# Kernel tuning notes

Hardware: AMD Instinct MI355X
Metric: run time of the kernel (lower is better)

The kernel has to match this reference:

```python
import math
import jax, jax.numpy as jnp
import numpy as np

T, B, E, H = 2048, 1, 2048, 32
HD = E // H          # head_dim = 64
HALF = HD // 2       # rotary half = 32
SCALE_LENGTH = 1024


def duplicate_interleave(m):
    # [S, HALF] -> [S, HD], each column duplicated adjacently
    return jnp.repeat(m, 2, axis=-1)


def rotate_every_two(x):
    # x: [BH, S, HD]
    x1 = x[:, :, ::2]
    x2 = x[:, :, 1::2]
    return jnp.stack((-x2, x1), axis=-1).reshape(x.shape)


def apply_rotary_pos_emb(x, sin, cos, scale):
    # sin/cos/scale: [S, HALF]; x: [BH, S, HD]
    sin2 = duplicate_interleave(sin * scale)
    cos2 = duplicate_interleave(cos * scale)
    return x * cos2 + rotate_every_two(x) * sin2


def setup_inputs() -> dict:
    key = jax.random.key(0)
    ks = jax.random.split(key, 8)
    std = 0.02
    query = jax.random.normal(ks[0], (T, B, E), jnp.float32)
    key_t = jax.random.normal(ks[1], (T, B, E), jnp.float32)
    value = jax.random.normal(ks[2], (T, B, E), jnp.float32)
    Wq = jax.random.normal(ks[3], (E, E), jnp.float32) * std
    Wk = jax.random.normal(ks[4], (E, E), jnp.float32) * std
    Wv = jax.random.normal(ks[5], (E, E), jnp.float32) * std
    Wo = jax.random.normal(ks[6], (E, E), jnp.float32) * std
    bq = jnp.zeros((E,), jnp.float32)
    bk = jnp.zeros((E,), jnp.float32)
    bv = jnp.zeros((E,), jnp.float32)
    bo = jnp.zeros((E,), jnp.float32)
    # XPos-style rotary tables
    pos = jnp.arange(T, dtype=jnp.float32)
    inv_freq = 1.0 / (10000.0 ** (jnp.arange(HALF, dtype=jnp.float32) / HALF))
    ang = pos[:, None] * inv_freq[None, :]          # [T, HALF]
    sin = jnp.sin(ang)
    cos = jnp.cos(ang)
    scale_base = 512.0
    dim_scale = (jnp.arange(0, HD, 2, dtype=jnp.float32) + 0.4 * HD) / (1.4 * HD)
    xscale = dim_scale[None, :] ** (pos[:, None] / scale_base)  # [T, HALF]
    # causal additive mask
    attn_mask = jnp.where(jnp.triu(jnp.ones((T, T), bool), k=1), -1e9, 0.0).astype(jnp.float32)
    return {"query": query, "key": key_t, "value": value,
            "Wq": Wq, "bq": bq, "Wk": Wk, "bk": bk, "Wv": Wv, "bv": bv,
            "Wo": Wo, "bo": bo, "sin": sin, "cos": cos, "xscale": xscale,
            "attn_mask": attn_mask, "scale_length": SCALE_LENGTH}


def reference(query, key, value, Wq, bq, Wk, bk, Wv, bv, Wo, bo,
              sin, cos, xscale, attn_mask, scale_length):
    tgt_len, bsz, embed_dim = query.shape
    scaling = HD ** -0.5

    def proj(x, W, b):
        y = x @ W.T + b                                # [T, B, E]
        return y.reshape(tgt_len, bsz * H, HD).transpose(1, 0, 2)  # [BH, T, HD]

    q = proj(query, Wq, bq)
    k = proj(key, Wk, bk)
    v = proj(value, Wv, bv)

    # self-attention XPos rotary: k scaled by 1/xscale, q by xscale (last q_len rows)
    k = apply_rotary_pos_emb(k, sin, cos, 1.0 / xscale)
    q = apply_rotary_pos_emb(q, sin[-tgt_len:], cos[-tgt_len:], xscale[-tgt_len:])

    src_len = k.shape[1]
    if src_len > scale_length:
        pos_k = jnp.arange(src_len - tgt_len, src_len, dtype=jnp.float32)
        scale_attention = jnp.maximum(1.0, jnp.log(pos_k) / math.log(scale_length))
        q = q * scale_attention[None, :, None]

    q = q * scaling
    attn_weights = jnp.einsum('btd,bsd->bts', q, k)      # [BH, T, S]
    attn_weights = attn_weights + attn_mask[None, :, :]
    attn_weights = jax.nn.softmax(attn_weights.astype(jnp.float32), axis=-1
                                  ).astype(q.dtype)
    attn = jnp.einsum('bts,bsd->btd', attn_weights, v)   # [BH, T, HD]
    attn = attn.transpose(1, 0, 2).reshape(tgt_len, bsz, embed_dim)
    attn = attn @ Wo.T + bo
    return attn
```

## Files before the change

### kernel.cpp

```cpp
#include <hip/hip_runtime.h>
#include <hip/hip_bf16.h>
#include <math.h>

#define T_LEN 2048
#define EMB   2048
#define NH    32
#define HD    64
#define HALF  32

typedef __attribute__((ext_vector_type(8))) short short8v;
typedef __attribute__((ext_vector_type(4))) float floatx4;

__device__ inline void gload_lds16(const void* g, void* l) {
    __builtin_amdgcn_global_load_lds(
        (const __attribute__((address_space(1))) unsigned int*)g,
        (__attribute__((address_space(3))) unsigned int*)l,
        16, 0, 0);
}

__device__ inline ushort f2bf(float x) {
    union { float f; unsigned u; } c; c.f = x;
    const unsigned r = c.u + 0x7FFFu + ((c.u >> 16) & 1u);
    return (ushort)(r >> 16);
}

#define BARRIER() do { asm volatile("" ::: "memory"); \
    __builtin_amdgcn_s_barrier(); asm volatile("" ::: "memory"); } while (0)
#define VMW4() asm volatile("s_waitcnt vmcnt(4)" ::: "memory")

__global__ __launch_bounds__(256) void conv_all(
    const float* __restrict__ s0, const float* __restrict__ s1,
    const float* __restrict__ s2, const float* __restrict__ s3,
    const float* __restrict__ s4, const float* __restrict__ s5,
    const float* __restrict__ s6, ushort* __restrict__ dst)
{
    const int idx = blockIdx.x * 256 + threadIdx.x;
    const int t = idx >> 19;
    const int r = (idx & 524287) * 8;
    const float* in = t == 0 ? s0 : t == 1 ? s1 : t == 2 ? s2 : t == 3 ? s3
                    : t == 4 ? s4 : t == 5 ? s5 : s6;
    const float4 v0 = *reinterpret_cast<const float4*>(&in[r]);
    const float4 v1 = *reinterpret_cast<const float4*>(&in[r + 4]);
    ushort o[8];
    o[0] = f2bf(v0.x); o[1] = f2bf(v0.y); o[2] = f2bf(v0.z); o[3] = f2bf(v0.w);
    o[4] = f2bf(v1.x); o[5] = f2bf(v1.y); o[6] = f2bf(v1.z); o[7] = f2bf(v1.w);
    *reinterpret_cast<uint4*>(&dst[(size_t)t * 4194304 + r]) =
        *reinterpret_cast<const uint4*>(o);
}

__global__ __launch_bounds__(256) void rot_tables(
    const float* __restrict__ sinp, const float* __restrict__ cosp,
    const float* __restrict__ xscale,
    float2* __restrict__ qt, float2* __restrict__ kt)
{
    const int idx = blockIdx.x * 256 + threadIdx.x;
    const int t = idx >> 5;
    const float s = sinp[idx], c = cosp[idx], xs = xscale[idx];
    float sa = 1.f;
    if (t >= 2) {
        const float lv = __logf((float)t) * 0.14426950408889634f;
        sa = lv > 1.f ? lv : 1.f;
    }
    const float qs = xs * sa * 0.125f * 1.4426950408889634f;
    qt[idx] = make_float2(c * qs, s * qs);
    const float ks = 1.f / xs;
    kt[idx] = make_float2(c * ks, s * ks);
}

#define QBM 256
#define QBN 256

#define STAGE_A(tau, h) do {                                                   \
    const int _tc = ((tau) & 31) * 64;                                         \
    _Pragma("unroll") for (int _i = 0; _i < 2; ++_i) {                         \
        gload_lds16(&Ap[(size_t)(bm + (h) * 128 + wid * 16 + _i * 8 + rl) * 2048 + _tc + csw], \
                    &lds[((tau) & 1) * 16384 + (h) * 8192 + (wid * 16 + _i * 8) * 64]); \
    } } while (0)

#define STAGE_B(tau, h) do {                                                   \
    const int _tc = ((tau) & 31) * 64;                                         \
    _Pragma("unroll") for (int _i = 0; _i < 2; ++_i) {                         \
        gload_lds16(&Bp[(size_t)(bn + (h) * 128 + wid * 16 + _i * 8 + rl) * 2048 + _tc + csw], \
                    &lds[32768 + ((tau) & 1) * 16384 + (h) * 8192 + (wid * 16 + _i * 8) * 64]); \
    } } while (0)

#define PH(slot, mp, VMWSTMT, ...) do {                                        \
    if ((mp) == 0) {                                                           \
        _Pragma("unroll") for (int n = 0; n < 4; ++n) {                        \
            bf[n][0] = ldB(slot, n, 0);                                        \
            bf[n][1] = ldB(slot, n, 1);                                        \
        }                                                                      \
    }                                                                          \
    af[0][0] = ldA(slot, (mp) * 2, 0);     af[0][1] = ldA(slot, (mp) * 2, 1);  \
    af[1][0] = ldA(slot, (mp) * 2 + 1, 0); af[1][1] = ldA(slot, (mp) * 2 + 1, 1); \
    __VA_ARGS__;                                                               \
    BARRIER();                                                                 \
    __builtin_amdgcn_s_setprio(1);                                             \
    _Pragma("unroll") for (int mm = 0; mm < 2; ++mm)                           \
    _Pragma("unroll") for (int n = 0; n < 4; ++n)                              \
    _Pragma("unroll") for (int kk = 0; kk < 2; ++kk)                           \
        acc[(mp) * 2 + mm][n] = __builtin_amdgcn_mfma_f32_16x16x32_bf16(       \
            af[mm][kk], bf[n][kk], acc[(mp) * 2 + mm][n], 0, 0, 0);            \
    __builtin_amdgcn_s_setprio(0);                                             \
    VMWSTMT;                                                                   \
    BARRIER();                                                                 \
} while (0)

__global__ __launch_bounds__(512, 2) void gemm_qkv8(
    const ushort* __restrict__ Astack,
    const ushort* __restrict__ Wstack,
    const float* __restrict__ bq, const float* __restrict__ bk,
    const float* __restrict__ bv,
    ushort* __restrict__ outQ, ushort* __restrict__ outK,
    ushort* __restrict__ outVt,
    const float2* __restrict__ qtab, const float2* __restrict__ ktab)
{
    __shared__ ushort lds[65536];
    const int tid  = threadIdx.x;
    const int lane = tid & 63;
    const int wid  = tid >> 6;

    const int b   = blockIdx.x + blockIdx.y * 24;
    const int xcd = b & 7;
    const int idx = b >> 3;
    const int bx  = xcd * 3 + (idx >> 3);
    const int by  = idx & 7;
    const int which = bx >> 3;
    const int bn  = (bx & 7) * QBN;
    const int bm  = by * QBM;
    const ushort* Ap = Astack + (size_t)which * 4194304;
    const ushort* Bp = Wstack + (size_t)which * 4194304;

    const int rl  = lane >> 3;
    const int csw = (((lane & 7) ^ ((lane >> 3) & 7)) * 8);
    const int lm  = lane & 15;
    const int lg  = lane >> 4;
    const char* ldsb = reinterpret_cast<const char*>(lds);

    auto ldA = [&](int slot, int m, int kk) -> short8v {
        const int row = m * 16 + lm;
        const int off = (slot * 16384 + (wid >> 2) * 8192) * 2 + row * 128
                      + (((kk * 4 + lg) ^ (row & 7)) * 16);
        return *reinterpret_cast<const short8v*>(ldsb + off);
    };
    auto ldB = [&](int slot, int n, int kk) -> short8v {
        const int row = (wid & 1) * 64 + n * 16 + lm;
        const int off = (32768 + slot * 16384 + ((wid & 3) >> 1) * 8192) * 2
                      + row * 128 + (((kk * 4 + lg) ^ (row & 7)) * 16);
        return *reinterpret_cast<const short8v*>(ldsb + off);
    };

    floatx4 acc[8][4] = {};
    short8v bf[4][2];
    short8v af[2][2];

    STAGE_A(0, 0); STAGE_A(0, 1);
    STAGE_B(0, 0); STAGE_B(0, 1);
    STAGE_B(1, 0); STAGE_B(1, 1);
    VMW4();
    BARRIER();

    for (int i = 0; i < 16; ++i) {
        const int t = 2 * i;
        PH(0, 0, (void)0, STAGE_A(t + 1, 0));
        PH(0, 1, (void)0, STAGE_A(t + 1, 1));
        PH(0, 2, (void)0, STAGE_B(t + 2, 0));
        PH(0, 3, VMW4(),  STAGE_B(t + 2, 1));
        PH(1, 0, (void)0, STAGE_A(t + 2, 0));
        PH(1, 1, (void)0, STAGE_A(t + 2, 1));
        PH(1, 2, (void)0, STAGE_B(t + 3, 0));
        PH(1, 3, VMW4(),  STAGE_B(t + 3, 1));
    }
    asm volatile("s_waitcnt vmcnt(0)" ::: "memory");

    const float* bias = which == 0 ? bq : which == 1 ? bk : bv;
    const float2* tbl = which == 0 ? qtab : ktab;
    #pragma unroll
    for (int m = 0; m < 8; ++m) {
        #pragma unroll
        for (int n = 0; n < 4; ++n) {
            const int col = bn + (wid & 3) * 64 + n * 16 + lm;
            const float bz = bias[col];
            const int row0 = bm + (wid >> 2) * 128 + m * 16 + lg * 4;
            if (which == 2) {
                ushort o4[4];
                #pragma unroll
                for (int j = 0; j < 4; ++j)
                    o4[j] = f2bf(acc[m][n][j] + bz);
                *reinterpret_cast<uint2*>(&outVt[(size_t)col * T_LEN + row0]) =
                    *reinterpret_cast<const uint2*>(o4);
            } else {
                ushort* O = which == 0 ? outQ : outK;
                const int p = (col & 63) >> 1;
                const bool even = (col & 1) == 0;
                #pragma unroll
                for (int j = 0; j < 4; ++j) {
                    const int row = row0 + j;
                    const float v = acc[m][n][j] + bz;
                    const float pv = __shfl_xor(v, 1);
                    const float2 cs = tbl[row * HALF + p];
                    const float outv = even ? v * cs.x - pv * cs.y
                                            : v * cs.x + pv * cs.y;
                    O[(size_t)row * EMB + col] = f2bf(outv);
                }
            }
        }
    }
}

#define GBM 128
#define GBN 128
#define GBK 64

__global__ __launch_bounds__(256) void gemm_out_sk(
    const ushort* __restrict__ A,
    const ushort* __restrict__ B,
    float* __restrict__ P)
{
    __shared__ ushort As[GBM * GBK];
    __shared__ ushort Bs[GBN * GBK];
    const int tid  = threadIdx.x;
    const int lane = tid & 63;
    const int wid  = tid >> 6;
    const int bm = blockIdx.y * GBM;
    const int bn = blockIdx.x * GBN;
    const int z  = blockIdx.z;
    const int wr = (wid >> 1) * 64;
    const int wc = (wid & 1) * 64;

    floatx4 acc[4][4] = {};

    const int lrow  = lane >> 3;
    const int lcolb = (lane & 7) * 8;

    for (int k0 = z * 1024; k0 < (z + 1) * 1024; k0 += GBK) {
        #pragma unroll
        for (int c = 0; c < 4; ++c) {
            const int chunk = wid * 4 + c;
            const int row = chunk * 8 + lrow;
            gload_lds16(&A[(size_t)(bm + row) * EMB + k0 + lcolb], &As[chunk * 512]);
            gload_lds16(&B[(size_t)(bn + row) * EMB + k0 + lcolb], &Bs[chunk * 512]);
        }
        __syncthreads();
        #pragma unroll
        for (int kk = 0; kk < 2; ++kk) {
            short8v a[4], b[4];
            #pragma unroll
            for (int m = 0; m < 4; ++m)
                a[m] = *reinterpret_cast<const short8v*>(
                    &As[(wr + m * 16 + (lane & 15)) * GBK + kk * 32 + (lane >> 4) * 8]);
            #pragma unroll
            for (int n = 0; n < 4; ++n)
                b[n] = *reinterpret_cast<const short8v*>(
                    &Bs[(wc + n * 16 + (lane & 15)) * GBK + kk * 32 + (lane >> 4) * 8]);
            #pragma unroll
            for (int m = 0; m < 4; ++m)
                #pragma unroll
                for (int n = 0; n < 4; ++n)
                    acc[m][n] = __builtin_amdgcn_mfma_f32_16x16x32_bf16(
                        a[m], b[n], acc[m][n], 0, 0, 0);
        }
        __syncthreads();
    }

    float* Pz = P + (size_t)z * 4194304;
    const int cr = (lane >> 4) * 4;
    const int cc = lane & 15;
    #pragma unroll
    for (int m = 0; m < 4; ++m) {
        #pragma unroll
        for (int n = 0; n < 4; ++n) {
            const int col = bn + wc + n * 16 + cc;
            #pragma unroll
            for (int j = 0; j < 4; ++j) {
                const int row = bm + wr + m * 16 + cr + j;
                Pz[(size_t)row * EMB + col] = acc[m][n][j];
            }
        }
    }
}

__global__ __launch_bounds__(256) void reduce_out(
    const float* __restrict__ P, const float* __restrict__ bias,
    float* __restrict__ C)
{
    const int i = (blockIdx.x * 256 + threadIdx.x) * 4;
    const float4 a = *reinterpret_cast<const float4*>(&P[i]);
    const float4 b = *reinterpret_cast<const float4*>(&P[4194304 + i]);
    const float4 bz = *reinterpret_cast<const float4*>(&bias[i & 2047]);
    float4 o;
    o.x = a.x + b.x + bz.x; o.y = a.y + b.y + bz.y;
    o.z = a.z + b.z + bz.z; o.w = a.w + b.w + bz.w;
    *reinterpret_cast<float4*>(&C[i]) = o;
}

__global__ __launch_bounds__(256) void flash_attn_mfma(
    const ushort* __restrict__ Qb,
    const ushort* __restrict__ Kb,
    const ushort* __restrict__ Vt,
    ushort* __restrict__ Ob)
{
    __shared__ ushort Ks[2][64 * 64];
    __shared__ ushort Vs[2][64 * 64];
    __shared__ ushort Ps[4][16 * 64];

    const int h   = blockIdx.x;
    const int qb  = (T_LEN / 64 - 1) - blockIdx.y;
    const int tid = threadIdx.x;
    const int lane = tid & 63;
    const int wid  = tid >> 6;
    const int qrow_w = qb * 64 + wid * 16;
    const int lm = lane & 15;
    const int lg = lane >> 4;

    short8v qf[2];
    {
        const ushort* qp = &Qb[(size_t)(qrow_w + lm) * EMB + h * HD + lg * 8];
        qf[0] = *reinterpret_cast<const short8v*>(qp);
        qf[1] = *reinterpret_cast<const short8v*>(qp + 32);
    }

    floatx4 oacc[4] = {};
    float m = -1e30f, l = 0.f;

    const int srow = lane >> 3;
    const int schk = lane & 7;

    {
        #pragma unroll
        for (int i = 0; i < 2; ++i) {
            const int slot = wid * 2 + i;
            const int row  = slot * 8 + srow;
            const int cswz = (schk ^ (row & 7)) * 8;
            gload_lds16(&Kb[(size_t)row * EMB + h * HD + cswz], &Ks[0][slot * 512]);
            gload_lds16(&Vt[(size_t)(h * HD + row) * T_LEN + cswz], &Vs[0][slot * 512]);
        }
    }
    __syncthreads();

    for (int kb = 0; kb <= qb; ++kb) {
        const int cur = kb & 1;
        if (kb < qb) {
            const int nkb = kb + 1;
            #pragma unroll
            for (int i = 0; i < 2; ++i) {
                const int slot = wid * 2 + i;
                const int row  = slot * 8 + srow;
                const int cswz = (schk ^ (row & 7)) * 8;
                gload_lds16(&Kb[(size_t)(nkb * 64 + row) * EMB + h * HD + cswz],
                            &Ks[cur ^ 1][slot * 512]);
                gload_lds16(&Vt[(size_t)(h * HD + row) * T_LEN + nkb * 64 + cswz],
                            &Vs[cur ^ 1][slot * 512]);
            }
        }

        float sv[16];
        #pragma unroll
        for (int t = 0; t < 4; ++t) {
            floatx4 sacc = {};
            const int srow_l = t * 16 + lm;
            const char* krow = reinterpret_cast<const char*>(Ks[cur]) + srow_l * 128;
            const int swz = (srow_l & 7) << 4;
            #pragma unroll
            for (int kk = 0; kk < 2; ++kk) {
                const int cb = (kk * 64 + lg * 16) ^ swz;
                short8v kf = *reinterpret_cast<const short8v*>(krow + cb);
                sacc = __builtin_amdgcn_mfma_f32_16x16x32_bf16(kf, qf[kk], sacc, 0, 0, 0);
            }
            sv[t * 4 + 0] = sacc[0]; sv[t * 4 + 1] = sacc[1];
            sv[t * 4 + 2] = sacc[2]; sv[t * 4 + 3] = sacc[3];
        }

        const int qg = qrow_w + lm;
        if (kb == qb) {
            #pragma unroll
            for (int t = 0; t < 4; ++t)
                #pragma unroll
                for (int r = 0; r < 4; ++r) {
                    const int sg = kb * 64 + t * 16 + lg * 4 + r;
                    if (sg > qg) sv[t * 4 + r] = -1e30f;
                }
        }

        float mx = sv[0];
        #pragma unroll
        for (int i = 1; i < 16; ++i) mx = fmaxf(mx, sv[i]);
        mx = fmaxf(mx, __shfl_xor(mx, 16));
        mx = fmaxf(mx, __shfl_xor(mx, 32));
        float corr = 1.f;
        if (!__all(mx - m <= 11.544f)) {
            const float mnew = fmaxf(m, mx);
            corr = exp2f(m - mnew);
            m = mnew;
            float corr4[4];
            #pragma unroll
            for (int r = 0; r < 4; ++r)
                corr4[r] = __shfl(corr, lg * 4 + r);
            #pragma unroll
            for (int td = 0; td < 4; ++td)
                #pragma unroll
                for (int r = 0; r < 4; ++r)
                    oacc[td][r] *= corr4[r];
        }
        float ps = 0.f;
        unsigned pw[8];
        #pragma unroll
        for (int i = 0; i < 8; ++i) {
            const float p0 = exp2f(sv[2 * i + 0] - m);
            const float p1 = exp2f(sv[2 * i + 1] - m);
            ps += p0 + p1;
            const __hip_bfloat162 h2 = __float22bfloat162_rn(make_float2(p0, p1));
            pw[i] = *reinterpret_cast<const unsigned*>(&h2);
        }
        ps += __shfl_xor(ps, 16);
        ps += __shfl_xor(ps, 32);
        l = l * corr + ps;

        {
            char* pbase = reinterpret_cast<char*>(&Ps[wid][0]) + lm * 128;
            const int swz = (lm & 7) << 4;
            #pragma unroll
            for (int t = 0; t < 4; ++t) {
                uint2 w;
                w.x = pw[2 * t + 0];
                w.y = pw[2 * t + 1];
                const int cb = (t * 32 + lg * 8) ^ swz;
                *reinterpret_cast<uint2*>(pbase + cb) = w;
            }
        }

        const char* pwave = reinterpret_cast<const char*>(&Ps[wid][0]);
        #pragma unroll
        for (int kk = 0; kk < 2; ++kk) {
            const int acb = (kk * 64 + lg * 16) ^ ((lm & 7) << 4);
            short8v pa = *reinterpret_cast<const short8v*>(pwave + lm * 128 + acb);
            #pragma unroll
            for (int td = 0; td < 4; ++td) {
                const int d = td * 16 + lm;
                const int bcb = (kk * 64 + lg * 16) ^ ((d & 7) << 4);
                short8v vb = *reinterpret_cast<const short8v*>(
                    reinterpret_cast<const char*>(Vs[cur]) + d * 128 + bcb);
                oacc[td] = __builtin_amdgcn_mfma_f32_16x16x32_bf16(pa, vb, oacc[td], 0, 0, 0);
            }
        }

        __syncthreads();
    }

    float invl[4];
    #pragma unroll
    for (int r = 0; r < 4; ++r)
        invl[r] = 1.f / __shfl(l, lg * 4 + r);
    #pragma unroll
    for (int td = 0; td < 4; ++td) {
        #pragma unroll
        for (int r = 0; r < 4; ++r) {
            const int trow = qrow_w + lg * 4 + r;
            const int col  = h * HD + td * 16 + lm;
            Ob[(size_t)trow * EMB + col] = f2bf(oacc[td][r] * invl[r]);
        }
    }
}

extern "C" void kernel_launch(void* const* d_in, const int* in_sizes, int n_in,
                              void* d_out, int out_size, void* d_ws, size_t ws_size,
                              hipStream_t stream) {
    const float* query = (const float*)d_in[0];
    const float* key   = (const float*)d_in[1];
    const float* value = (const float*)d_in[2];
    const float* Wq = (const float*)d_in[3];
    const float* bq = (const float*)d_in[4];
    const float* Wk = (const float*)d_in[5];
    const float* bk = (const float*)d_in[6];
    const float* Wv = (const float*)d_in[7];
    const float* bv = (const float*)d_in[8];
    const float* Wo = (const float*)d_in[9];
    const float* bo = (const float*)d_in[10];
    const float* sinp   = (const float*)d_in[11];
    const float* cosp   = (const float*)d_in[12];
    const float* xscale = (const float*)d_in[13];
    float* out = (float*)d_out;

    const size_t MB = 1024 * 1024;
    char* ws = (char*)d_ws;
    ushort* bWqkv = (ushort*)(ws + 0 * MB);
    ushort* bWo   = (ushort*)(ws + 24 * MB);
    ushort* bAqkv = (ushort*)(ws + 32 * MB);
    ushort* bQ  = (ushort*)(ws + 56 * MB);
    ushort* bK  = (ushort*)(ws + 64 * MB);
    ushort* bVt = (ushort*)(ws + 72 * MB);
    ushort* bAo = (ushort*)(ws + 80 * MB);
    float2* qtab = (float2*)(ws + 88 * MB);
    float2* ktab = (float2*)(ws + 88 * MB + 512 * 1024);
    float*  Pout = (float*)(ws + 32 * MB);

    conv_all<<<7 * 524288 / 256, 256, 0, stream>>>(
        Wq, Wk, Wv, Wo, query, key, value, bWqkv);
    rot_tables<<<T_LEN * HALF / 256, 256, 0, stream>>>(
        sinp, cosp, xscale, qtab, ktab);

    dim3 gQKV(24, 8);
    gemm_qkv8<<<gQKV, 512, 0, stream>>>(bAqkv, bWqkv, bq, bk, bv,
                                        bQ, bK, bVt, qtab, ktab);

    dim3 gFlash(NH, T_LEN / 64);
    flash_attn_mfma<<<gFlash, 256, 0, stream>>>(bQ, bK, bVt, bAo);

    dim3 gOut(EMB / GBN, T_LEN / GBM, 2);
    gemm_out_sk<<<gOut, 256, 0, stream>>>(bAo, bWo, Pout);
    reduce_out<<<T_LEN * EMB / (256 * 4), 256, 0, stream>>>(Pout, bo, out);
}
```

Baseline: 175.9 us.

## Triple-buffer A tiles in LDS to deepen QKV GEMM prefetch

Reworks the QKV projection GEMM's main loop so A tiles rotate through three LDS slots while B tiles keep two. A tiles are prefetched two k-steps ahead, and the wait threshold is relaxed to vmcnt(8). The loop is unrolled into six-tile groups, followed by an explicit two-tile tail. The aim is to hide more global-load latency behind the MFMA phases. In exchange the kernel uses 160KB of LDS, which may limit occupancy, and the slot rotation is more complex.

```diff
diff --git a/kernel.cpp b/kernel.cpp
--- a/kernel.cpp
+++ b/kernel.cpp
@@ -26,7 +26,9 @@
 
 #define BARRIER() do { asm volatile("" ::: "memory"); \
     __builtin_amdgcn_s_barrier(); asm volatile("" ::: "memory"); } while (0)
+#define VMW8() asm volatile("s_waitcnt vmcnt(8)" ::: "memory")
 #define VMW4() asm volatile("s_waitcnt vmcnt(4)" ::: "memory")
+#define VMW0() asm volatile("s_waitcnt vmcnt(0)" ::: "memory")
 
 __global__ __launch_bounds__(256) void conv_all(
     const float* __restrict__ s0, const float* __restrict__ s1,
@@ -70,29 +72,29 @@
 #define QBM 256
 #define QBN 256
 
-#define STAGE_A(tau, h) do {                                                   \
-    const int _tc = ((tau) & 31) * 64;                                         \
+#define STAGE_A3(tau, h, slot) do {                                            \
+    const int _tc = (tau) * 64;                                                \
     _Pragma("unroll") for (int _i = 0; _i < 2; ++_i) {                         \
         gload_lds16(&Ap[(size_t)(bm + (h) * 128 + wid * 16 + _i * 8 + rl) * 2048 + _tc + csw], \
-                    &lds[((tau) & 1) * 16384 + (h) * 8192 + (wid * 16 + _i * 8) * 64]); \
+                    &lds[(slot) * 16384 + (h) * 8192 + (wid * 16 + _i * 8) * 64]); \
     } } while (0)
 
-#define STAGE_B(tau, h) do {                                                   \
-    const int _tc = ((tau) & 31) * 64;                                         \
+#define STAGE_B2(tau, h, slot) do {                                            \
+    const int _tc = (tau) * 64;                                                \
     _Pragma("unroll") for (int _i = 0; _i < 2; ++_i) {                         \
         gload_lds16(&Bp[(size_t)(bn + (h) * 128 + wid * 16 + _i * 8 + rl) * 2048 + _tc + csw], \
-                    &lds[32768 + ((tau) & 1) * 16384 + (h) * 8192 + (wid * 16 + _i * 8) * 64]); \
+                    &lds[49152 + (slot) * 16384 + (h) * 8192 + (wid * 16 + _i * 8) * 64]); \
     } } while (0)
 
-#define PH(slot, mp, VMWSTMT, ...) do {                                        \
+#define PH(sa_, sb_, mp, VMWSTMT, ...) do {                                    \
     if ((mp) == 0) {                                                           \
         _Pragma("unroll") for (int n = 0; n < 4; ++n) {                        \
-            bf[n][0] = ldB(slot, n, 0);                                        \
-            bf[n][1] = ldB(slot, n, 1);                                        \
+            bf[n][0] = ldB(sb_, n, 0);                                         \
+            bf[n][1] = ldB(sb_, n, 1);                                         \
         }                                                                      \
     }                                                                          \
-    af[0][0] = ldA(slot, (mp) * 2, 0);     af[0][1] = ldA(slot, (mp) * 2, 1);  \
-    af[1][0] = ldA(slot, (mp) * 2 + 1, 0); af[1][1] = ldA(slot, (mp) * 2 + 1, 1); \
+    af[0][0] = ldA(sa_, (mp) * 2, 0);     af[0][1] = ldA(sa_, (mp) * 2, 1);    \
+    af[1][0] = ldA(sa_, (mp) * 2 + 1, 0); af[1][1] = ldA(sa_, (mp) * 2 + 1, 1);\
     __VA_ARGS__;                                                               \
     BARRIER();                                                                 \
     __builtin_amdgcn_s_setprio(1);                                             \
@@ -106,6 +108,13 @@
     BARRIER();                                                                 \
 } while (0)
 
+#define TILE6(sa, sb, sa2, tau2, LASTVMW) do {                                 \
+    PH(sa, sb, 0, (void)0, STAGE_A3(tau2, 0, sa2));                            \
+    PH(sa, sb, 1, (void)0, STAGE_A3(tau2, 1, sa2));                            \
+    PH(sa, sb, 2, (void)0, STAGE_B2(tau2, 0, sb));                             \
+    PH(sa, sb, 3, LASTVMW, STAGE_B2(tau2, 1, sb));                             \
+} while (0)
+
 __global__ __launch_bounds__(512, 2) void gemm_qkv8(
     const ushort* __restrict__ Astack,
     const ushort* __restrict__ Wstack,
@@ -115,7 +124,7 @@
     ushort* __restrict__ outVt,
     const float2* __restrict__ qtab, const float2* __restrict__ ktab)
 {
-    __shared__ ushort lds[65536];
+    __shared__ ushort lds[81920];
     const int tid  = threadIdx.x;
     const int lane = tid & 63;
     const int wid  = tid >> 6;
@@ -145,7 +154,7 @@
     };
     auto ldB = [&](int slot, int n, int kk) -> short8v {
         const int row = (wid & 1) * 64 + n * 16 + lm;
-        const int off = (32768 + slot * 16384 + ((wid & 3) >> 1) * 8192) * 2
+        const int off = (49152 + slot * 16384 + ((wid & 3) >> 1) * 8192) * 2
                       + row * 128 + (((kk * 4 + lg) ^ (row & 7)) * 16);
         return *reinterpret_cast<const short8v*>(ldsb + off);
     };
@@ -154,24 +163,30 @@
     short8v bf[4][2];
     short8v af[2][2];
 
-    STAGE_A(0, 0); STAGE_A(0, 1);
-    STAGE_B(0, 0); STAGE_B(0, 1);
-    STAGE_B(1, 0); STAGE_B(1, 1);
-    VMW4();
+    STAGE_A3(0, 0, 0); STAGE_A3(0, 1, 0);
+    STAGE_B2(0, 0, 0); STAGE_B2(0, 1, 0);
+    STAGE_A3(1, 0, 1); STAGE_A3(1, 1, 1);
+    STAGE_B2(1, 0, 1); STAGE_B2(1, 1, 1);
+    VMW8();
     BARRIER();
 
-    for (int i = 0; i < 16; ++i) {
-        const int t = 2 * i;
-        PH(0, 0, (void)0, STAGE_A(t + 1, 0));
-        PH(0, 1, (void)0, STAGE_A(t + 1, 1));
-        PH(0, 2, (void)0, STAGE_B(t + 2, 0));
-        PH(0, 3, VMW4(),  STAGE_B(t + 2, 1));
-        PH(1, 0, (void)0, STAGE_A(t + 2, 0));
-        PH(1, 1, (void)0, STAGE_A(t + 2, 1));
-        PH(1, 2, (void)0, STAGE_B(t + 3, 0));
-        PH(1, 3, VMW4(),  STAGE_B(t + 3, 1));
-    }
-    asm volatile("s_waitcnt vmcnt(0)" ::: "memory");
+    for (int i = 0; i < 5; ++i) {
+        const int t = 6 * i;
+        TILE6(0, 0, 2, t + 2, VMW8());
+        TILE6(1, 1, 0, t + 3, VMW8());
+        TILE6(2, 0, 1, t + 4, VMW8());
+        TILE6(0, 1, 2, t + 5, VMW8());
+        TILE6(1, 0, 0, t + 6, VMW8());
+        TILE6(2, 1, 1, t + 7, VMW8());
+    }
+    PH(0, 0, 0, (void)0, (void)0);
+    PH(0, 0, 1, (void)0, (void)0);
+    PH(0, 0, 2, (void)0, (void)0);
+    PH(0, 0, 3, VMW0(),  (void)0);
+    PH(1, 1, 0, (void)0, (void)0);
+    PH(1, 1, 1, (void)0, (void)0);
+    PH(1, 1, 2, (void)0, (void)0);
+    PH(1, 1, 3, (void)0, (void)0);
 
     const float* bias = which == 0 ? bq : which == 1 ? bk : bv;
     const float2* tbl = which == 0 ? qtab : ktab;
```

Measured after the change: 175.7 us. Within noise of the previous version (-0.1%).
